# Optimization experiments

Measured on AMD Instinct MI355X. Metric: run time of the kernel, lower is better.

## Reference

```python
import jax, jax.numpy as jnp
import numpy as np

B, L, K, D, S = 8, 1024, 1024, 128, 16  # batch, nodes, eigvecs, d_model(=d_inner), d_state
ABAR_EPS = 1e-3
BN_EPS = 1e-5


def setup_inputs() -> dict:
    key = jax.random.key(0)
    ks = jax.random.split(key, 10)
    x = jax.random.normal(ks[0], (B, L, D), jnp.float32)
    attn_mask = jnp.ones((B, L), jnp.bool_)
    EigVecs = jax.random.normal(ks[1], (B, L, K), jnp.float32)
    EigVals = jax.random.uniform(ks[2], (B, K), jnp.float32)
    # BatchNorm1d (eval mode) params
    bn_gamma = jnp.ones((D,), jnp.float32)
    bn_beta = jnp.zeros((D,), jnp.float32)
    bn_mean = jnp.zeros((D,), jnp.float32)
    bn_var = jnp.ones((D,), jnp.float32)
    # in_proj Linear(D, 2*D)
    W_in = jax.random.normal(ks[3], (D, 2 * D), jnp.float32) / np.float32(np.sqrt(D))
    b_in = jnp.zeros((2 * D,), jnp.float32)
    # SSM params
    log_Delta = np.float32(np.log(1e-3)) + np.float32(np.log(0.1) - np.log(1e-3)) * jax.random.uniform(ks[4], (1, D), jnp.float32)
    Bp = 0.01 * jax.random.normal(ks[5], (1, D, S), jnp.float32)
    Cp = 0.01 * jax.random.normal(ks[6], (1, D, S), jnp.float32)
    log_A_real = jnp.log(0.5 * jnp.ones((D, S), jnp.float32))
    A_imag = jnp.pi * jnp.broadcast_to(jnp.arange(D, dtype=jnp.float32)[:, None], (D, S))
    # out_proj Linear(D, D)
    W_out = jax.random.normal(ks[7], (D, D), jnp.float32) / np.float32(np.sqrt(D))
    b_out = jnp.zeros((D,), jnp.float32)
    return {
        "x": x, "attn_mask": attn_mask, "EigVecs": EigVecs, "EigVals": EigVals,
        "bn_gamma": bn_gamma, "bn_beta": bn_beta, "bn_mean": bn_mean, "bn_var": bn_var,
        "W_in": W_in, "b_in": b_in, "log_Delta": log_Delta, "Bp": Bp, "Cp": Cp,
        "log_A_real": log_A_real, "A_imag": A_imag, "W_out": W_out, "b_out": b_out,
    }


def reference(x, attn_mask, EigVecs, EigVals, bn_gamma, bn_beta, bn_mean, bn_var,
              W_in, b_in, log_Delta, Bp, Cp, log_A_real, A_imag, W_out, b_out):
    # --- eig preprocessing ---
    ev = 1.0 - EigVals[:, :, None, None]            # (B,K,1,1)
    ev = jnp.nan_to_num(ev)
    Q = jnp.nan_to_num(EigVecs)                      # (B,L,K)
    Q = Q / jnp.linalg.norm(Q, axis=-1, keepdims=True)
    Q = jnp.nan_to_num(Q)
    # --- in_proj: BatchNorm1d (eval) + Linear ---
    xb = (x - bn_mean) * (bn_gamma / jnp.sqrt(bn_var + BN_EPS)) + bn_beta
    h = xb @ W_in + b_in                             # (B,L,2D)
    x1, z = jnp.split(h, 2, axis=-1)                 # split [d_model, d_model]
    u = x1 * jax.nn.silu(z)                          # (B,L,D)
    # --- discretized SSM params ---
    delta = jnp.exp(log_Delta)                       # (1,D)
    A = -jnp.exp(log_A_real) + 1j * A_imag           # (D,S) complex
    Abar = jnp.exp(-ABAR_EPS + delta[..., None] * A) # (1,D,S) complex
    Bbar = delta[..., None] * Bp                     # (1,D,S)
    # --- graph Fourier transform ---
    QTX = jnp.einsum('blk,bld->bkd', Q, u)           # (B,K,D)
    QTXB = QTX[..., None] * Bbar                     # (B,K,D,S)
    lamA = ev * Abar[:, None]                        # (B,K,D,S) complex
    lamQ = jnp.real(lamA / (1.0 - lamA) * QTXB)      # A_complex & not BC_complex -> .real
    # --- inverse transform + C reduction (fused) ---
    yssm = jnp.einsum('blk,bkds,ds->bld', Q, lamQ, Cp[0])  # (B,L,D)
    y = jax.nn.silu(yssm) @ W_out + b_out
    return y
```

## Files before the change

kernel.cpp:

```cpp
#include <hip/hip_runtime.h>
#include <math.h>

#define B_ 8
#define L_ 1024
#define K_ 1024
#define D_ 128
#define S_ 16
#define DS_ (D_ * S_)
#define NIT_ 16

typedef short bf16x8 __attribute__((ext_vector_type(8)));
typedef float f32x4 __attribute__((ext_vector_type(4)));
typedef __attribute__((address_space(1))) const unsigned int gu32;
typedef __attribute__((address_space(3))) unsigned int lu32;

__device__ inline unsigned short f2bf(float f) {
    unsigned int u = __float_as_uint(f);
    u = (u + 0x7fffu + ((u >> 16) & 1u)) >> 16;
    return (unsigned short)u;
}
__device__ inline float bf2f(unsigned short h) {
    return __uint_as_float(((unsigned int)h) << 16);
}

__device__ inline size_t bswz(int b, int c, int n) {
    return ((((size_t)b * 32 + (c >> 5)) * 4 + ((c >> 3) & 3)) * 128 + n) * 8;
}

__global__ __launch_bounds__(256) void k_pre(
    const float* __restrict__ E, const float* __restrict__ x,
    const float* __restrict__ g, const float* __restrict__ beta,
    const float* __restrict__ mean, const float* __restrict__ var,
    const float* __restrict__ W_in, const float* __restrict__ b_in,
    const float* __restrict__ log_Delta, const float* __restrict__ Bp,
    const float* __restrict__ Cp, const float* __restrict__ log_A_real,
    const float* __restrict__ A_imag,
    float* __restrict__ rn_out, float* __restrict__ par,
    unsigned short* __restrict__ uswH, unsigned short* __restrict__ uswL) {
    __shared__ float xb[16][128];
    __shared__ float rsum[16];
    __shared__ float rnS[16];
    int bx = blockIdx.x;
    int row0 = bx * 16;
    int t = threadIdx.x;
    if (bx < 8) {
        int i = bx * 256 + t;
        int d = i >> 4, s = i & 15;
        double delta = exp((double)log_Delta[d]);
        double Are = -exp((double)log_A_real[i]);
        double Aim = (double)A_imag[i];
        double mag = exp(-1e-3 + delta * Are);
        double ang = delta * Aim;
        int o = s * D_ + d;
        par[o]           = (float)(mag * cos(ang));
        par[DS_ + o]     = (float)(mag * sin(ang));
        par[2 * DS_ + o] = (float)(delta * (double)Bp[i] * (double)Cp[i]);
    }
    {
        int r = t >> 4, tt = t & 15;
        const float4* Ep = (const float4*)(E + (size_t)(row0 + r) * K_);
        float s = 0.f;
        #pragma unroll
        for (int i = 0; i < 16; ++i) {
            float4 v = Ep[tt + i * 16];
            s += v.x * v.x + v.y * v.y + v.z * v.z + v.w * v.w;
        }
        s += __shfl_xor(s, 8, 64);
        s += __shfl_xor(s, 4, 64);
        s += __shfl_xor(s, 2, 64);
        s += __shfl_xor(s, 1, 64);
        if (tt == 0) rsum[r] = s;
    }
    #pragma unroll
    for (int p = 0; p < 8; ++p) {
        int idx = t + p * 256;
        int dd = idx & 127, r = idx >> 7;
        float sc = g[dd] / sqrtf(var[dd] + 1e-5f);
        xb[r][dd] = (x[(size_t)(row0 + r) * D_ + dd] - mean[dd]) * sc + beta[dd];
    }
    __syncthreads();
    if (t < 16) {
        float rv = 1.0f / sqrtf(rsum[t]);
        rnS[t] = rv;
        rn_out[row0 + t] = rv;
    }
    __syncthreads();
    int j = t & 127, half = t >> 7;
    float acc1[8], acc2[8];
    #pragma unroll
    for (int r = 0; r < 8; ++r) { acc1[r] = 0.f; acc2[r] = 0.f; }
    #pragma unroll 4
    for (int dd = 0; dd < 128; ++dd) {
        float w1 = W_in[dd * 256 + j];
        float w2 = W_in[dd * 256 + 128 + j];
        #pragma unroll
        for (int r = 0; r < 8; ++r) {
            float xv = xb[half * 8 + r][dd];
            acc1[r] = fmaf(xv, w1, acc1[r]);
            acc2[r] = fmaf(xv, w2, acc2[r]);
        }
    }
    float b1 = b_in[j], b2 = b_in[128 + j];
    bf16x8 hv, lv;
    #pragma unroll
    for (int r = 0; r < 8; ++r) {
        int rr = half * 8 + r;
        float x1 = acc1[r] + b1;
        float z  = acc2[r] + b2;
        float sig = 1.0f / (1.0f + __expf(-z));
        float uv = rnS[rr] * x1 * z * sig;
        unsigned short h = f2bf(uv);
        hv[r] = (short)h;
        lv[r] = (short)f2bf(uv - bf2f(h));
    }
    int b = row0 >> 10;
    int l0 = (row0 & 1023) + half * 8;
    size_t off = bswz(b, l0, j);
    *(bf16x8*)&uswH[off] = hv;
    *(bf16x8*)&uswL[off] = lv;
}

#define STAGE_B(itS, nb)                                                        \
    _Pragma("unroll")                                                           \
    for (int j2 = 0; j2 < 4; ++j2) {                                            \
        int s = wave * 4 + j2;                         \
        int cts = s >> 4, s2 = s & 15;                                          \
        int qq = s2 & 3, nh = (s2 >> 2) & 1, hl = s2 >> 3;                      \
        size_t src0 = (size_t)((itS) * 2 + cts) * 4096;                         \
        const unsigned short* src =                                             \
            (hl ? BbL : BbH) + src0 + ((size_t)qq * 128 + nh * 64 + lane) * 8;  \
        unsigned short* dst =                                                   \
            (hl ? &sBl[nb][cts][0] : &sBh[nb][cts][0]) + qq * 1032 + nh * 512;  \
        __builtin_amdgcn_global_load_lds((gu32*)src, (lu32*)dst, 16, 0, 0);     \
    }

#define G1_WRITE_A(nb, v0, v1, v2, v3)                                           \
    {                                                                            \
        unsigned short h0 = f2bf(v0), h1 = f2bf(v1);                             \
        unsigned short l0 = f2bf((v0) - bf2f(h0)), l1 = f2bf((v1) - bf2f(h1));   \
        *(unsigned int*)&sAh[nb][0][aoff] = (unsigned)h0 | ((unsigned)h1 << 16); \
        *(unsigned int*)&sAl[nb][0][aoff] = (unsigned)l0 | ((unsigned)l1 << 16); \
        unsigned short h2 = f2bf(v2), h3 = f2bf(v3);                             \
        unsigned short l2 = f2bf((v2) - bf2f(h2)), l3 = f2bf((v3) - bf2f(h3));   \
        *(unsigned int*)&sAh[nb][1][aoff] = (unsigned)h2 | ((unsigned)h3 << 16); \
        *(unsigned int*)&sAl[nb][1][aoff] = (unsigned)l2 | ((unsigned)l3 << 16); \
    }

#define MFMA_PHASE(aB, cB)                                                       \
    __builtin_amdgcn_s_setprio(1);                                               \
    _Pragma("unroll")                                                            \
    for (int ks = 0; ks < 2; ++ks) {                                             \
        bf16x8 ah, al, bh[2], bl[2];                                             \
        {                                                                        \
            int row = wm * 16 + fr;                                              \
            int p = (q + (row >> 3)) & 3;                                        \
            int offA = row * 40 + p * 8;                                         \
            ah = *(const bf16x8*)&sAh[aB][ks][offA];                             \
            al = *(const bf16x8*)&sAl[aB][ks][offA];                             \
        }                                                                        \
        _Pragma("unroll")                                                        \
        for (int nt = 0; nt < 2; ++nt) {                                         \
            int offB = q * 1032 + (wn + nt * 16 + fr) * 8;                       \
            bh[nt] = *(const bf16x8*)&sBh[cB][ks][offB];                         \
            bl[nt] = *(const bf16x8*)&sBl[cB][ks][offB];                         \
        }                                                                        \
        _Pragma("unroll")                                                        \
        for (int nt = 0; nt < 2; ++nt) {                                         \
            acc[nt] = __builtin_amdgcn_mfma_f32_16x16x32_bf16(ah, bh[nt], acc[nt], 0, 0, 0); \
            acc[nt] = __builtin_amdgcn_mfma_f32_16x16x32_bf16(ah, bl[nt], acc[nt], 0, 0, 0); \
            acc[nt] = __builtin_amdgcn_mfma_f32_16x16x32_bf16(al, bh[nt], acc[nt], 0, 0, 0); \
        }                                                                        \
    }                                                                            \
    __builtin_amdgcn_s_setprio(0);

__global__ __launch_bounds__(512, 2) void k_g1(
    const float* __restrict__ E,
    const unsigned short* __restrict__ BH, const unsigned short* __restrict__ BL,
    const float* __restrict__ EigVals, const float* __restrict__ par,
    unsigned short* __restrict__ GswH, unsigned short* __restrict__ GswL) {
    __shared__ alignas(16) unsigned short sAh[2][2][1280], sAl[2][2][1280];
    __shared__ alignas(16) unsigned short sBh[3][2][4128], sBl[3][2][4128];
    __shared__ float evS[32];
    int bx = blockIdx.x;
    int b = bx & 7;
    int m0 = (bx >> 3) * 32;
    const float* Ab = E + (size_t)b * (1024 * 1024);
    const unsigned short* BbH = BH + (size_t)b * 131072;
    const unsigned short* BbL = BL + (size_t)b * 131072;
    int t = threadIdx.x;
    int wave = t >> 6, lane = t & 63;
    int fr = lane & 15, q = lane >> 4;
    int wm = wave & 1;
    int wn = (wave >> 1) * 32;
    int am = t & 31, jj = t >> 5;
    int ag = jj >> 2;
    int arot = (ag + (am >> 3)) & 3;
    int aoff = am * 40 + arot * 8 + ((2 * jj) & 7);
    if (t < 32) evS[t] = 1.0f - EigVals[b * 1024 + m0 + t];
    f32x4 acc[2];
    acc[0] = (f32x4){0.f, 0.f, 0.f, 0.f};
    acc[1] = (f32x4){0.f, 0.f, 0.f, 0.f};

    {
        STAGE_B(0, 0);
        STAGE_B(1, 1);
        float v0 = Ab[(size_t)(2 * jj) * 1024 + m0 + am];
        float v1 = Ab[(size_t)(2 * jj + 1) * 1024 + m0 + am];
        float v2 = Ab[(size_t)(32 + 2 * jj) * 1024 + m0 + am];
        float v3 = Ab[(size_t)(32 + 2 * jj + 1) * 1024 + m0 + am];
        G1_WRITE_A(0, v0, v1, v2, v3);
        asm volatile("s_waitcnt vmcnt(0) lgkmcnt(0)" ::: "memory");
        __builtin_amdgcn_s_barrier();
        asm volatile("" ::: "memory");
    }

    for (int it = 0; it < NIT_; ++it) {
        int cB = it % 3;
        int fB = (it + 2) % 3;
        int aB = it & 1, naB = aB ^ 1;
        float v0 = 0.f, v1 = 0.f, v2 = 0.f, v3 = 0.f;
        if (it + 1 < NIT_) {
            int cb = (it + 1) * 64;
            v0 = Ab[(size_t)(cb + 2 * jj) * 1024 + m0 + am];
            v1 = Ab[(size_t)(cb + 2 * jj + 1) * 1024 + m0 + am];
            v2 = Ab[(size_t)(cb + 32 + 2 * jj) * 1024 + m0 + am];
            v3 = Ab[(size_t)(cb + 32 + 2 * jj + 1) * 1024 + m0 + am];
        }
        if (it + 2 < NIT_) STAGE_B(it + 2, fB);
        MFMA_PHASE(aB, cB)
        if (it + 1 < NIT_) G1_WRITE_A(naB, v0, v1, v2, v3);
        asm volatile("s_waitcnt lgkmcnt(0)" ::: "memory");
        __builtin_amdgcn_s_barrier();
        asm volatile("" ::: "memory");
    }

    float (*Gs)[132] = (float (*)[132])(&sBh[0][0][0]);
    #pragma unroll
    for (int nt = 0; nt < 2; ++nt) {
        int col = wn + nt * 16 + fr;
        #pragma unroll
        for (int r = 0; r < 4; ++r)
            Gs[wm * 16 + q * 4 + r][col] = acc[nt][r];
    }
    __syncthreads();
    {
        int col = t & 127, rowg = t >> 7;
        float arr[S_], aii[S_], ccc[S_];
        #pragma unroll
        for (int ss = 0; ss < S_; ++ss) {
            arr[ss] = par[ss * D_ + col];
            aii[ss] = par[DS_ + ss * D_ + col];
            ccc[ss] = par[2 * DS_ + ss * D_ + col];
        }
        #pragma unroll
        for (int i = 0; i < 8; ++i) {
            int row = rowg * 8 + i;
            float ev = evS[row];
            float w = 0.f;
            #pragma unroll
            for (int ss = 0; ss < S_; ++ss) {
                float a = ev * arr[ss], bi = ev * aii[ss];
                float oma = 1.0f - a;
                float b2 = bi * bi;
                float num = fmaf(a, oma, -b2);
                float den = fmaf(oma, oma, b2);
                float rr = __builtin_amdgcn_rcpf(den);
                rr = rr * (2.0f - den * rr);
                w = fmaf(ccc[ss], num * rr, w);
            }
            Gs[row][col] *= w;
        }
    }
    __syncthreads();
    {
        int d = t & 127, kg = t >> 7;
        bf16x8 hv, lv;
        #pragma unroll
        for (int i = 0; i < 8; ++i) {
            float v = Gs[kg * 8 + i][d];
            unsigned short h = f2bf(v);
            hv[i] = (short)h;
            lv[i] = (short)f2bf(v - bf2f(h));
        }
        int ct = m0 >> 5;
        size_t off = (((size_t)(b * 32 + ct) * 4 + kg) * 128 + d) * 8;
        *(bf16x8*)&GswH[off] = hv;
        *(bf16x8*)&GswL[off] = lv;
    }
}

#define G2_WRITE_A(nb, va)                                                       \
    {                                                                            \
        unsigned short h0 = f2bf((va).x), h1 = f2bf((va).y);                     \
        unsigned short h2 = f2bf((va).z), h3 = f2bf((va).w);                     \
        unsigned short l0 = f2bf((va).x - bf2f(h0)), l1 = f2bf((va).y - bf2f(h1));\
        unsigned short l2 = f2bf((va).z - bf2f(h2)), l3 = f2bf((va).w - bf2f(h3));\
        *(uint2*)&sAh[nb][chunk][aoff] =                                         \
            (uint2){(unsigned)h0 | ((unsigned)h1 << 16),                         \
                    (unsigned)h2 | ((unsigned)h3 << 16)};                        \
        *(uint2*)&sAl[nb][chunk][aoff] =                                         \
            (uint2){(unsigned)l0 | ((unsigned)l1 << 16),                         \
                    (unsigned)l2 | ((unsigned)l3 << 16)};                        \
    }

__global__ __launch_bounds__(512, 2) void k_g2(
    const float* __restrict__ E,
    const unsigned short* __restrict__ BH, const unsigned short* __restrict__ BL,
    const float* __restrict__ rn, const float* __restrict__ W_out,
    const float* __restrict__ b_out, float* __restrict__ y) {
    __shared__ alignas(16) unsigned short sAh[2][2][1280], sAl[2][2][1280];
    __shared__ alignas(16) unsigned short sBh[3][2][4128], sBl[3][2][4128];
    __shared__ float rnS[32];
    int bx = blockIdx.x;
    int b = bx & 7;
    int m0 = (bx >> 3) * 32;
    const float* Ab = E + (size_t)b * (1024 * 1024);
    const unsigned short* BbH = BH + (size_t)b * 131072;
    const unsigned short* BbL = BL + (size_t)b * 131072;
    int t = threadIdx.x;
    int wave = t >> 6, lane = t & 63;
    int fr = lane & 15, q = lane >> 4;
    int wm = wave & 1;
    int wn = (wave >> 1) * 32;
    int am = t >> 4, c4 = (t & 15) * 4;
    int chunk = c4 >> 5, cw = c4 & 31;
    int ag = cw >> 3;
    int arot = (ag + (am >> 3)) & 3;
    int aoff = am * 40 + arot * 8 + (cw & 7);
    if (t < 32) rnS[t] = rn[b * 1024 + m0 + t];
    f32x4 acc[2];
    acc[0] = (f32x4){0.f, 0.f, 0.f, 0.f};
    acc[1] = (f32x4){0.f, 0.f, 0.f, 0.f};

    {
        STAGE_B(0, 0);
        STAGE_B(1, 1);
        float4 va = *(const float4*)&Ab[(size_t)(m0 + am) * 1024 + c4];
        G2_WRITE_A(0, va);
        asm volatile("s_waitcnt vmcnt(0) lgkmcnt(0)" ::: "memory");
        __builtin_amdgcn_s_barrier();
        asm volatile("" ::: "memory");
    }

    for (int it = 0; it < NIT_; ++it) {
        int cB = it % 3;
        int fB = (it + 2) % 3;
        int aB = it & 1, naB = aB ^ 1;
        float4 va = (float4){0.f, 0.f, 0.f, 0.f};
        if (it + 1 < NIT_)
            va = *(const float4*)&Ab[(size_t)(m0 + am) * 1024 + (it + 1) * 64 + c4];
        if (it + 2 < NIT_) STAGE_B(it + 2, fB);
        MFMA_PHASE(aB, cB)
        if (it + 1 < NIT_) G2_WRITE_A(naB, va);
        asm volatile("s_waitcnt lgkmcnt(0)" ::: "memory");
        __builtin_amdgcn_s_barrier();
        asm volatile("" ::: "memory");
    }

    float (*Ys)[132] = (float (*)[132])(&sBh[0][0][0]);
    #pragma unroll
    for (int nt = 0; nt < 2; ++nt) {
        int col = wn + nt * 16 + fr;
        #pragma unroll
        for (int r = 0; r < 4; ++r) {
            int row = wm * 16 + q * 4 + r;
            float v = acc[nt][r] * rnS[row];
            float sig = 1.0f / (1.0f + __expf(-v));
            Ys[row][col] = v * sig;
        }
    }
    __syncthreads();
    int j = t & 127, h = t >> 7;
    float a2[8];
    #pragma unroll
    for (int r = 0; r < 8; ++r) a2[r] = 0.f;
    for (int dd = 0; dd < 128; dd += 4) {
        float w0 = W_out[(dd + 0) * 128 + j];
        float w1 = W_out[(dd + 1) * 128 + j];
        float w2 = W_out[(dd + 2) * 128 + j];
        float w3 = W_out[(dd + 3) * 128 + j];
        #pragma unroll
        for (int r = 0; r < 8; ++r) {
            float4 yv = *(float4*)&Ys[h * 8 + r][dd];
            a2[r] = fmaf(yv.x, w0, a2[r]);
            a2[r] = fmaf(yv.y, w1, a2[r]);
            a2[r] = fmaf(yv.z, w2, a2[r]);
            a2[r] = fmaf(yv.w, w3, a2[r]);
        }
    }
    float bo = b_out[j];
    #pragma unroll
    for (int r = 0; r < 8; ++r)
        y[((size_t)b * 1024 + m0 + h * 8 + r) * 128 + j] = a2[r] + bo;
}

extern "C" void kernel_launch(void* const* d_in, const int* in_sizes, int n_in,
                              void* d_out, int out_size, void* d_ws, size_t ws_size,
                              hipStream_t stream) {
    const float* x          = (const float*)d_in[0];
    const float* EigVecs    = (const float*)d_in[2];
    const float* EigVals    = (const float*)d_in[3];
    const float* bn_gamma   = (const float*)d_in[4];
    const float* bn_beta    = (const float*)d_in[5];
    const float* bn_mean    = (const float*)d_in[6];
    const float* bn_var     = (const float*)d_in[7];
    const float* W_in       = (const float*)d_in[8];
    const float* b_in       = (const float*)d_in[9];
    const float* log_Delta  = (const float*)d_in[10];
    const float* Bp         = (const float*)d_in[11];
    const float* Cp         = (const float*)d_in[12];
    const float* log_A_real = (const float*)d_in[13];
    const float* A_imag     = (const float*)d_in[14];
    const float* W_out      = (const float*)d_in[15];
    const float* b_out      = (const float*)d_in[16];

    float* y = (float*)d_out;
    char* w = (char*)d_ws;
    float* rn            = (float*)(w);
    float* par           = (float*)(w + 32768);
    unsigned short* uswH = (unsigned short*)(w + 65536);
    unsigned short* uswL = (unsigned short*)(w + 65536 + (1u << 21));
    unsigned short* GswH = (unsigned short*)(w + 65536 + 2 * (1u << 21));
    unsigned short* GswL = (unsigned short*)(w + 65536 + 3 * (1u << 21));

    k_pre<<<dim3(B_ * L_ / 16), dim3(256), 0, stream>>>(
        EigVecs, x, bn_gamma, bn_beta, bn_mean, bn_var, W_in, b_in,
        log_Delta, Bp, Cp, log_A_real, A_imag, rn, par, uswH, uswL);
    k_g1<<<dim3(256), dim3(512), 0, stream>>>(
        EigVecs, uswH, uswL, EigVals, par, GswH, GswL);
    k_g2<<<dim3(256), dim3(512), 0, stream>>>(
        EigVecs, GswH, GswL, rn, W_out, b_out, y);
}
```

Baseline: 164.0 us.

## Split K across wave pairs instead of M in g1/g2 MFMA phase

Changes the wave work split in both GEMM kernels. Each wave now covers both 16-row M tiles and one of the two K halves, where before each wave covered one M tile and both K halves. The goal is to reuse each B fragment load across two M tiles, halving B LDS reads per MFMA. In exchange, accumulator registers double and an extra LDS reduction pass with barriers is needed to combine the two K-half partial sums.

Measured after the change: 163.5 us. No clear change (-0.3%).

```diff
diff --git a/kernel.cpp b/kernel.cpp
--- a/kernel.cpp
+++ b/kernel.cpp
@@ -147,31 +147,33 @@
     }
 
 #define MFMA_PHASE(aB, cB)                                                       \
-    __builtin_amdgcn_s_setprio(1);                                               \
-    _Pragma("unroll")                                                            \
-    for (int ks = 0; ks < 2; ++ks) {                                             \
-        bf16x8 ah, al, bh[2], bl[2];                                             \
-        {                                                                        \
-            int row = wm * 16 + fr;                                              \
+    {                                                                            \
+        __builtin_amdgcn_s_setprio(1);                                           \
+        bf16x8 ah[2], al[2], bh[2], bl[2];                                       \
+        _Pragma("unroll")                                                        \
+        for (int mt = 0; mt < 2; ++mt) {                                         \
+            int row = mt * 16 + fr;                                              \
             int p = (q + (row >> 3)) & 3;                                        \
             int offA = row * 40 + p * 8;                                         \
-            ah = *(const bf16x8*)&sAh[aB][ks][offA];                             \
-            al = *(const bf16x8*)&sAl[aB][ks][offA];                             \
+            ah[mt] = *(const bf16x8*)&sAh[aB][kh][offA];                         \
+            al[mt] = *(const bf16x8*)&sAl[aB][kh][offA];                         \
         }                                                                        \
         _Pragma("unroll")                                                        \
         for (int nt = 0; nt < 2; ++nt) {                                         \
             int offB = q * 1032 + (wn + nt * 16 + fr) * 8;                       \
-            bh[nt] = *(const bf16x8*)&sBh[cB][ks][offB];                         \
-            bl[nt] = *(const bf16x8*)&sBl[cB][ks][offB];                         \
+            bh[nt] = *(const bf16x8*)&sBh[cB][kh][offB];                         \
+            bl[nt] = *(const bf16x8*)&sBl[cB][kh][offB];                         \
         }                                                                        \
         _Pragma("unroll")                                                        \
-        for (int nt = 0; nt < 2; ++nt) {                                         \
-            acc[nt] = __builtin_amdgcn_mfma_f32_16x16x32_bf16(ah, bh[nt], acc[nt], 0, 0, 0); \
-            acc[nt] = __builtin_amdgcn_mfma_f32_16x16x32_bf16(ah, bl[nt], acc[nt], 0, 0, 0); \
-            acc[nt] = __builtin_amdgcn_mfma_f32_16x16x32_bf16(al, bh[nt], acc[nt], 0, 0, 0); \
-        }                                                                        \
-    }                                                                            \
-    __builtin_amdgcn_s_setprio(0);
+        for (int mt = 0; mt < 2; ++mt)                                           \
+            _Pragma("unroll")                                                    \
+            for (int nt = 0; nt < 2; ++nt) {                                     \
+                acc[mt][nt] = __builtin_amdgcn_mfma_f32_16x16x32_bf16(ah[mt], bh[nt], acc[mt][nt], 0, 0, 0); \
+                acc[mt][nt] = __builtin_amdgcn_mfma_f32_16x16x32_bf16(ah[mt], bl[nt], acc[mt][nt], 0, 0, 0); \
+                acc[mt][nt] = __builtin_amdgcn_mfma_f32_16x16x32_bf16(al[mt], bh[nt], acc[mt][nt], 0, 0, 0); \
+            }                                                                    \
+        __builtin_amdgcn_s_setprio(0);                                           \
+    }
 
 __global__ __launch_bounds__(512, 2) void k_g1(
     const float* __restrict__ E,
@@ -190,16 +192,19 @@
     int t = threadIdx.x;
     int wave = t >> 6, lane = t & 63;
     int fr = lane & 15, q = lane >> 4;
-    int wm = wave & 1;
+    int kh = wave & 1;
     int wn = (wave >> 1) * 32;
     int am = t & 31, jj = t >> 5;
     int ag = jj >> 2;
     int arot = (ag + (am >> 3)) & 3;
     int aoff = am * 40 + arot * 8 + ((2 * jj) & 7);
     if (t < 32) evS[t] = 1.0f - EigVals[b * 1024 + m0 + t];
-    f32x4 acc[2];
-    acc[0] = (f32x4){0.f, 0.f, 0.f, 0.f};
-    acc[1] = (f32x4){0.f, 0.f, 0.f, 0.f};
+    f32x4 acc[2][2];
+    #pragma unroll
+    for (int mt = 0; mt < 2; ++mt)
+        #pragma unroll
+        for (int nt = 0; nt < 2; ++nt)
+            acc[mt][nt] = (f32x4){0.f, 0.f, 0.f, 0.f};
 
     {
         STAGE_B(0, 0);
@@ -235,12 +240,28 @@
     }
 
     float (*Gs)[132] = (float (*)[132])(&sBh[0][0][0]);
-    #pragma unroll
-    for (int nt = 0; nt < 2; ++nt) {
-        int col = wn + nt * 16 + fr;
-        #pragma unroll
-        for (int r = 0; r < 4; ++r)
-            Gs[wm * 16 + q * 4 + r][col] = acc[nt][r];
+    if (kh == 0) {
+        #pragma unroll
+        for (int mt = 0; mt < 2; ++mt)
+            #pragma unroll
+            for (int nt = 0; nt < 2; ++nt) {
+                int col = wn + nt * 16 + fr;
+                #pragma unroll
+                for (int r = 0; r < 4; ++r)
+                    Gs[mt * 16 + q * 4 + r][col] = acc[mt][nt][r];
+            }
+    }
+    __syncthreads();
+    if (kh == 1) {
+        #pragma unroll
+        for (int mt = 0; mt < 2; ++mt)
+            #pragma unroll
+            for (int nt = 0; nt < 2; ++nt) {
+                int col = wn + nt * 16 + fr;
+                #pragma unroll
+                for (int r = 0; r < 4; ++r)
+                    Gs[mt * 16 + q * 4 + r][col] += acc[mt][nt][r];
+            }
     }
     __syncthreads();
     {
@@ -320,7 +341,7 @@
     int t = threadIdx.x;
     int wave = t >> 6, lane = t & 63;
     int fr = lane & 15, q = lane >> 4;
-    int wm = wave & 1;
+    int kh = wave & 1;
     int wn = (wave >> 1) * 32;
     int am = t >> 4, c4 = (t & 15) * 4;
     int chunk = c4 >> 5, cw = c4 & 31;
@@ -328,9 +349,12 @@
     int arot = (ag + (am >> 3)) & 3;
     int aoff = am * 40 + arot * 8 + (cw & 7);
     if (t < 32) rnS[t] = rn[b * 1024 + m0 + t];
-    f32x4 acc[2];
-    acc[0] = (f32x4){0.f, 0.f, 0.f, 0.f};
-    acc[1] = (f32x4){0.f, 0.f, 0.f, 0.f};
+    f32x4 acc[2][2];
+    #pragma unroll
+    for (int mt = 0; mt < 2; ++mt)
+        #pragma unroll
+        for (int nt = 0; nt < 2; ++nt)
+            acc[mt][nt] = (f32x4){0.f, 0.f, 0.f, 0.f};
 
     {
         STAGE_B(0, 0);
@@ -358,13 +382,36 @@
     }
 
     float (*Ys)[132] = (float (*)[132])(&sBh[0][0][0]);
-    #pragma unroll
-    for (int nt = 0; nt < 2; ++nt) {
-        int col = wn + nt * 16 + fr;
-        #pragma unroll
-        for (int r = 0; r < 4; ++r) {
-            int row = wm * 16 + q * 4 + r;
-            float v = acc[nt][r] * rnS[row];
+    if (kh == 0) {
+        #pragma unroll
+        for (int mt = 0; mt < 2; ++mt)
+            #pragma unroll
+            for (int nt = 0; nt < 2; ++nt) {
+                int col = wn + nt * 16 + fr;
+                #pragma unroll
+                for (int r = 0; r < 4; ++r)
+                    Ys[mt * 16 + q * 4 + r][col] = acc[mt][nt][r];
+            }
+    }
+    __syncthreads();
+    if (kh == 1) {
+        #pragma unroll
+        for (int mt = 0; mt < 2; ++mt)
+            #pragma unroll
+            for (int nt = 0; nt < 2; ++nt) {
+                int col = wn + nt * 16 + fr;
+                #pragma unroll
+                for (int r = 0; r < 4; ++r)
+                    Ys[mt * 16 + q * 4 + r][col] += acc[mt][nt][r];
+            }
+    }
+    __syncthreads();
+    {
+        int col = t & 127, rowg = t >> 7;
+        #pragma unroll
+        for (int i = 0; i < 8; ++i) {
+            int row = rowg * 8 + i;
+            float v = Ys[row][col] * rnS[row];
             float sig = 1.0f / (1.0f + __expf(-v));
             Ys[row][col] = v * sig;
         }
```
